# Kernel tuning notes

Hardware: AMD Instinct MI355X
Metric: run time of the kernel (lower is better)

## Reference

```python
import jax, jax.numpy as jnp
import numpy as np

H = 1024
V = 50257
L = 4096

def setup_inputs() -> dict:
    key = jax.random.key(0)
    ks = jax.random.split(key, 10)
    s = 1.0 / np.sqrt(H)
    return {
        "input": jax.random.randint(ks[0], (1,), 0, V, dtype=jnp.int64),
        "hidden": jax.random.normal(ks[1], (1, 1, H), dtype=jnp.float32),
        "encoder_hiddens": jax.random.normal(ks[2], (L, H), dtype=jnp.float32),
        "embedding": jax.random.normal(ks[3], (V, H), dtype=jnp.float32),
        "w_ih": jax.random.uniform(ks[4], (3 * H, H), minval=-s, maxval=s, dtype=jnp.float32),
        "w_hh": jax.random.uniform(ks[5], (3 * H, H), minval=-s, maxval=s, dtype=jnp.float32),
        "b_ih": jax.random.uniform(ks[6], (3 * H,), minval=-s, maxval=s, dtype=jnp.float32),
        "b_hh": jax.random.uniform(ks[7], (3 * H,), minval=-s, maxval=s, dtype=jnp.float32),
        "out_w": jax.random.uniform(ks[8], (V, 2 * H), minval=-s, maxval=s, dtype=jnp.float32),
        "out_b": jax.random.uniform(ks[9], (V,), minval=-s, maxval=s, dtype=jnp.float32),
    }


def _gru_step(x, h, w_ih, w_hh, b_ih, b_hh):
    # x, h: (H,). PyTorch GRU cell gate math (gate order: r, z, n).
    gi = w_ih @ x + b_ih                      # (3H,)
    gh = w_hh @ h + b_hh                      # (3H,)
    i_r, i_z, i_n = gi[:H], gi[H:2 * H], gi[2 * H:]
    h_r, h_z, h_n = gh[:H], gh[H:2 * H], gh[2 * H:]
    r = jax.nn.sigmoid(i_r + h_r)
    z = jax.nn.sigmoid(i_z + h_z)
    n = jnp.tanh(i_n + r * h_n)
    return (1.0 - z) * n + z * h


def reference(input, hidden, encoder_hiddens, embedding, w_ih, w_hh, b_ih, b_hh, out_w, out_b):
    # Embedding lookup of single token -> (H,); dropout is identity at inference.
    x = embedding[input].reshape(-1)
    h = hidden[0, 0]                          # (H,)
    h_new = _gru_step(x, h, w_ih, w_hh, b_ih, b_hh)  # (H,)
    # Dot-product attention over encoder hiddens (L, H)
    scores = encoder_hiddens @ h_new          # (L,)
    attn = jax.nn.softmax(scores)             # (L,)
    ctx = attn @ encoder_hiddens              # (H,)
    concat = jnp.concatenate([ctx, h_new])    # (2H,)
    logits = out_w @ concat + out_b           # (V,)
    output = jax.nn.log_softmax(logits)[None, :]  # (1, V)
    return output, h_new[None, None, :]
```

## Files before the change

kernel.cpp:

```cpp
#include <hip/hip_runtime.h>
#include <hip/hip_bf16.h>

#define H 1024
#define V 50257
#define L 4096
#define CTXB 128
#define ROWS (L / CTXB)

__device__ __forceinline__ float sigmoidf_(float x) { return 1.f / (1.f + expf(-x)); }

__device__ __forceinline__ float dot4(float4 w, float4 c) {
    return w.x * c.x + w.y * c.y + w.z * c.z + w.w * c.w;
}

__global__ __launch_bounds__(64) void k_gru(const int* __restrict__ idx,
        const float* __restrict__ hidden, const float* __restrict__ emb,
        const float* __restrict__ w_ih, const float* __restrict__ w_hh,
        const float* __restrict__ b_ih, const float* __restrict__ b_hh,
        float* __restrict__ concat, float* __restrict__ out_h) {
    const int j = blockIdx.x;
    const int lane = threadIdx.x;
    const float* x   = emb + (size_t)idx[0] * H;
    const float* wir = w_ih + (size_t)j * H;
    const float* wiz = wir + (size_t)H * H;
    const float* win = wiz + (size_t)H * H;
    const float* whr = w_hh + (size_t)j * H;
    const float* whz = whr + (size_t)H * H;
    const float* whn = whz + (size_t)H * H;
    float sir = 0, siz = 0, sin_ = 0, shr = 0, shz = 0, shn = 0;
    #pragma unroll
    for (int it = 0; it < 4; ++it) {
        int elem = (it * 64 + lane) * 4;
        float4 xf = *(const float4*)(x + elem);
        float4 hf = *(const float4*)(hidden + elem);
        sir  += dot4(*(const float4*)(wir + elem), xf);
        siz  += dot4(*(const float4*)(wiz + elem), xf);
        sin_ += dot4(*(const float4*)(win + elem), xf);
        shr  += dot4(*(const float4*)(whr + elem), hf);
        shz  += dot4(*(const float4*)(whz + elem), hf);
        shn  += dot4(*(const float4*)(whn + elem), hf);
    }
    #pragma unroll
    for (int off = 32; off; off >>= 1) {
        sir += __shfl_xor(sir, off); siz += __shfl_xor(siz, off);
        sin_ += __shfl_xor(sin_, off); shr += __shfl_xor(shr, off);
        shz += __shfl_xor(shz, off); shn += __shfl_xor(shn, off);
    }
    if (lane == 0) {
        float r = sigmoidf_(sir + b_ih[j]       + shr + b_hh[j]);
        float z = sigmoidf_(siz + b_ih[H + j]   + shz + b_hh[H + j]);
        float n = tanhf(sin_ + b_ih[2*H + j] + r * (shn + b_hh[2*H + j]));
        float hn = (1.f - z) * n + z * hidden[j];
        concat[H + j] = hn;
        out_h[j] = hn;
    }
}

__global__ __launch_bounds__(256) void k_scores(const float* __restrict__ enc,
        const float* __restrict__ concat, float* __restrict__ scores) {
    const int wave = threadIdx.x >> 6, lane = threadIdx.x & 63;
    const int l = blockIdx.x * 4 + wave;
    const float* row = enc + (size_t)l * H;
    const float* h = concat + H;
    float s = 0.f;
    #pragma unroll
    for (int it = 0; it < 4; ++it) {
        int elem = (it * 64 + lane) * 4;
        s += dot4(*(const float4*)(row + elem), *(const float4*)(h + elem));
    }
    #pragma unroll
    for (int off = 32; off; off >>= 1) s += __shfl_xor(s, off);
    if (lane == 0) scores[l] = s;
}

__global__ __launch_bounds__(256) void k_softmax(const float* __restrict__ scores,
                                                 float* __restrict__ attn) {
    __shared__ float sm[8];
    const int t = threadIdx.x, lane = t & 63, wave = t >> 6;
    float v[16];
    float m = -INFINITY;
    #pragma unroll
    for (int i = 0; i < 16; ++i) { v[i] = scores[i * 256 + t]; m = fmaxf(m, v[i]); }
    #pragma unroll
    for (int off = 32; off; off >>= 1) m = fmaxf(m, __shfl_xor(m, off));
    if (lane == 0) sm[wave] = m;
    __syncthreads();
    m = fmaxf(fmaxf(sm[0], sm[1]), fmaxf(sm[2], sm[3]));
    float s = 0.f;
    #pragma unroll
    for (int i = 0; i < 16; ++i) { v[i] = expf(v[i] - m); s += v[i]; }
    #pragma unroll
    for (int off = 32; off; off >>= 1) s += __shfl_xor(s, off);
    __syncthreads();
    if (lane == 0) sm[wave] = s;
    __syncthreads();
    s = sm[0] + sm[1] + sm[2] + sm[3];
    float inv = 1.f / s;
    #pragma unroll
    for (int i = 0; i < 16; ++i) attn[i * 256 + t] = v[i] * inv;
}

__global__ __launch_bounds__(256) void k_ctx_partial(const float* __restrict__ enc,
        const float* __restrict__ attn, float* __restrict__ partial) {
    __shared__ float a[ROWS];
    const int t = threadIdx.x;
    const int r0 = blockIdx.x * ROWS;
    if (t < ROWS) a[t] = attn[r0 + t];
    __syncthreads();
    float acc0 = 0, acc1 = 0, acc2 = 0, acc3 = 0;
    const float* p = enc + (size_t)r0 * H + t * 4;
    #pragma unroll
    for (int l0 = 0; l0 < ROWS; l0 += 8) {
        float4 w[8];
        #pragma unroll
        for (int k = 0; k < 8; ++k) w[k] = *(const float4*)(p + (size_t)(l0 + k) * H);
        #pragma unroll
        for (int k = 0; k < 8; ++k) {
            float al = a[l0 + k];
            acc0 += al * w[k].x; acc1 += al * w[k].y;
            acc2 += al * w[k].z; acc3 += al * w[k].w;
        }
    }
    *(float4*)(partial + (size_t)blockIdx.x * H + t * 4) = make_float4(acc0, acc1, acc2, acc3);
}

__global__ __launch_bounds__(256) void k_ctx_reduce(const float* __restrict__ partial,
                                                    float* __restrict__ concat) {
    const int c = blockIdx.x * 256 + threadIdx.x;
    float s = 0.f;
    for (int p = 0; p < CTXB; ++p) s += partial[(size_t)p * H + c];
    concat[c] = s;
}

__global__ __launch_bounds__(256) void k_logits(const float* __restrict__ out_w,
        const float* __restrict__ out_b, const float* __restrict__ concat,
        float* __restrict__ logits) {
    const int wave = threadIdx.x >> 6, lane = threadIdx.x & 63;
    const int v = blockIdx.x * 4 + wave;
    if (v >= V) return;
    const float* row = out_w + (size_t)v * (2 * H);
    float s = 0.f;
    #pragma unroll
    for (int it = 0; it < 8; ++it) {
        int elem = (it * 64 + lane) * 4;
        s += dot4(*(const float4*)(row + elem), *(const float4*)(concat + elem));
    }
    #pragma unroll
    for (int off = 32; off; off >>= 1) s += __shfl_xor(s, off);
    if (lane == 0) logits[v] = s + out_b[v];
}

__global__ __launch_bounds__(256) void k_lse_partial(const float* __restrict__ logits,
                                                     float* __restrict__ red) {
    __shared__ float sm[4], ss[4];
    const int t = threadIdx.x;
    const int i = blockIdx.x * 256 + t;
    float m = -INFINITY, s = 0.f;
    for (int v = i; v < V; v += 64 * 256) {
        float x = logits[v];
        float M = fmaxf(m, x);
        s = s * expf(m - M) + expf(x - M);
        m = M;
    }
    const int lane = t & 63, wave = t >> 6;
    #pragma unroll
    for (int off = 32; off; off >>= 1) {
        float m2 = __shfl_xor(m, off), s2 = __shfl_xor(s, off);
        float M = fmaxf(m, m2);
        s = s * expf(m - M) + s2 * expf(m2 - M);
        m = M;
    }
    if (lane == 0) { sm[wave] = m; ss[wave] = s; }
    __syncthreads();
    if (t == 0) {
        float M = fmaxf(fmaxf(sm[0], sm[1]), fmaxf(sm[2], sm[3]));
        float S = ss[0] * expf(sm[0] - M) + ss[1] * expf(sm[1] - M) +
                  ss[2] * expf(sm[2] - M) + ss[3] * expf(sm[3] - M);
        red[blockIdx.x] = M;
        red[64 + blockIdx.x] = S;
    }
}

__global__ __launch_bounds__(256) void k_write(const float* __restrict__ logits,
        const float* __restrict__ red, float* __restrict__ out) {
    __shared__ float sC;
    const int t = threadIdx.x;
    if (t < 64) {
        float m = red[t], s = red[64 + t];
        #pragma unroll
        for (int off = 32; off; off >>= 1) {
            float m2 = __shfl_xor(m, off), s2 = __shfl_xor(s, off);
            float M = fmaxf(m, m2);
            s = s * expf(m - M) + s2 * expf(m2 - M);
            m = M;
        }
        if (t == 0) sC = m + logf(s);
    }
    __syncthreads();
    const float C = sC;
    const int v = blockIdx.x * 256 + t;
    if (v < V) out[v] = logits[v] - C;
}

extern "C" void kernel_launch(void* const* d_in, const int* in_sizes, int n_in,
                              void* d_out, int out_size, void* d_ws, size_t ws_size,
                              hipStream_t stream) {
    const int*   idx    = (const int*)d_in[0];
    const float* hidden = (const float*)d_in[1];
    const float* enc    = (const float*)d_in[2];
    const float* emb    = (const float*)d_in[3];
    const float* w_ih   = (const float*)d_in[4];
    const float* w_hh   = (const float*)d_in[5];
    const float* b_ih   = (const float*)d_in[6];
    const float* b_hh   = (const float*)d_in[7];
    const float* out_w  = (const float*)d_in[8];
    const float* out_b  = (const float*)d_in[9];
    float* out = (float*)d_out;

    float* ws      = (float*)d_ws;
    float* concat  = ws;
    float* scores  = ws + 2048;
    float* attn    = ws + 6144;
    float* partial = ws + 10240;
    float* logits  = ws + 141312;
    float* red     = ws + 191584;

    k_gru<<<H, 64, 0, stream>>>(idx, hidden, emb, w_ih, w_hh, b_ih, b_hh, concat, out + V);
    k_scores<<<L / 4, 256, 0, stream>>>(enc, concat, scores);
    k_softmax<<<1, 256, 0, stream>>>(scores, attn);
    k_ctx_partial<<<CTXB, 256, 0, stream>>>(enc, attn, partial);
    k_ctx_reduce<<<4, 256, 0, stream>>>(partial, concat);
    k_logits<<<(V + 3) / 4, 256, 0, stream>>>(out_w, out_b, concat, logits);
    k_lse_partial<<<64, 256, 0, stream>>>(logits, red);
    k_write<<<(V + 255) / 256, 256, 0, stream>>>(logits, red, out);
}
```

Baseline: 659.5 us.

## Fuse decoder step into one persistent cooperative kernel with grid syncs

The eight separate kernels (GRU, attention scores, softmax, context partial and reduce, logits, LSE partial, write) become one cooperative kernel of 256 blocks by 512 threads, with grid.sync between stages. The intent is to remove per-launch overhead and inter-kernel gaps. The logits pass also gains a per-wave online max/sum, so no separate pass is needed to compute log-sum-exp. The trade-off is lower occupancy, since the persistent grid has only 8 waves per block and each wave loops over many out_w rows, which may limit memory-level parallelism on the dominant output-projection stream.

```diff
diff --git a/kernel.cpp b/kernel.cpp
--- a/kernel.cpp
+++ b/kernel.cpp
@@ -1,11 +1,16 @@
 #include <hip/hip_runtime.h>
-#include <hip/hip_bf16.h>
+#include <hip/hip_cooperative_groups.h>
+
+namespace cg = cooperative_groups;
 
 #define H 1024
 #define V 50257
 #define L 4096
-#define CTXB 128
-#define ROWS (L / CTXB)
+#define NB 256
+#define NT 512
+#define NW 8
+#define GWAVES (NB * NW)
+#define ROWS2 (L / NB)
 
 __device__ __forceinline__ float sigmoidf_(float x) { return 1.f / (1.f + expf(-x)); }
 
@@ -13,193 +18,238 @@
     return w.x * c.x + w.y * c.y + w.z * c.z + w.w * c.w;
 }
 
-__global__ __launch_bounds__(64) void k_gru(const int* __restrict__ idx,
-        const float* __restrict__ hidden, const float* __restrict__ emb,
+__global__ __launch_bounds__(NT, 1) void k_mega(
+        const int* __restrict__ idx, const float* __restrict__ hidden,
+        const float* __restrict__ enc, const float* __restrict__ emb,
         const float* __restrict__ w_ih, const float* __restrict__ w_hh,
         const float* __restrict__ b_ih, const float* __restrict__ b_hh,
-        float* __restrict__ concat, float* __restrict__ out_h) {
-    const int j = blockIdx.x;
-    const int lane = threadIdx.x;
-    const float* x   = emb + (size_t)idx[0] * H;
-    const float* wir = w_ih + (size_t)j * H;
-    const float* wiz = wir + (size_t)H * H;
-    const float* win = wiz + (size_t)H * H;
-    const float* whr = w_hh + (size_t)j * H;
-    const float* whz = whr + (size_t)H * H;
-    const float* whn = whz + (size_t)H * H;
-    float sir = 0, siz = 0, sin_ = 0, shr = 0, shz = 0, shn = 0;
-    #pragma unroll
-    for (int it = 0; it < 4; ++it) {
-        int elem = (it * 64 + lane) * 4;
-        float4 xf = *(const float4*)(x + elem);
-        float4 hf = *(const float4*)(hidden + elem);
-        sir  += dot4(*(const float4*)(wir + elem), xf);
-        siz  += dot4(*(const float4*)(wiz + elem), xf);
-        sin_ += dot4(*(const float4*)(win + elem), xf);
-        shr  += dot4(*(const float4*)(whr + elem), hf);
-        shz  += dot4(*(const float4*)(whz + elem), hf);
-        shn  += dot4(*(const float4*)(whn + elem), hf);
-    }
-    #pragma unroll
-    for (int off = 32; off; off >>= 1) {
-        sir += __shfl_xor(sir, off); siz += __shfl_xor(siz, off);
-        sin_ += __shfl_xor(sin_, off); shr += __shfl_xor(shr, off);
-        shz += __shfl_xor(shz, off); shn += __shfl_xor(shn, off);
-    }
-    if (lane == 0) {
+        const float* __restrict__ out_w, const float* __restrict__ out_b,
+        float* __restrict__ out, float* __restrict__ ws) {
+    cg::grid_group grid = cg::this_grid();
+    const int t = threadIdx.x;
+    const int w = t >> 6, lane = t & 63;
+    const int bid = blockIdx.x;
+    const int gw = bid * NW + w;
+
+    float* concat  = ws;
+    float* scores  = ws + 2048;
+    float* Sb      = ws + 6144;
+    float* bmax    = ws + 6400;
+    float* red     = ws + 6656;
+    float* partial = ws + 8192;
+    float* logits  = ws + 8192 + NB * H;
+
+    __shared__ float gpart[NW][6];
+    __shared__ float wmax_s[NW];
+    __shared__ float eL[ROWS2];
+    __shared__ float aL[ROWS2];
+    __shared__ float mw[NW], sw[NW];
+    __shared__ float sScalar;
+
+    {
+        const int j = bid * 4 + (w >> 1);
+        const int half = w & 1;
+        const float* x   = emb + (size_t)idx[0] * H;
+        const float* wir = w_ih + (size_t)j * H;
+        const float* wiz = wir + (size_t)H * H;
+        const float* win = wiz + (size_t)H * H;
+        const float* whr = w_hh + (size_t)j * H;
+        const float* whz = whr + (size_t)H * H;
+        const float* whn = whz + (size_t)H * H;
+        float sir = 0, siz = 0, sin_ = 0, shr = 0, shz = 0, shn = 0;
+        #pragma unroll
+        for (int it = 0; it < 2; ++it) {
+            int elem = half * 512 + (it * 64 + lane) * 4;
+            float4 xf = *(const float4*)(x + elem);
+            float4 hf = *(const float4*)(hidden + elem);
+            sir  += dot4(*(const float4*)(wir + elem), xf);
+            siz  += dot4(*(const float4*)(wiz + elem), xf);
+            sin_ += dot4(*(const float4*)(win + elem), xf);
+            shr  += dot4(*(const float4*)(whr + elem), hf);
+            shz  += dot4(*(const float4*)(whz + elem), hf);
+            shn  += dot4(*(const float4*)(whn + elem), hf);
+        }
+        #pragma unroll
+        for (int off = 32; off; off >>= 1) {
+            sir += __shfl_xor(sir, off); siz += __shfl_xor(siz, off);
+            sin_ += __shfl_xor(sin_, off); shr += __shfl_xor(shr, off);
+            shz += __shfl_xor(shz, off); shn += __shfl_xor(shn, off);
+        }
+        if (lane == 0) {
+            gpart[w][0] = sir; gpart[w][1] = siz; gpart[w][2] = sin_;
+            gpart[w][3] = shr; gpart[w][4] = shz; gpart[w][5] = shn;
+        }
+    }
+    __syncthreads();
+    if (lane == 0 && (w & 1) == 0) {
+        const int j = bid * 4 + (w >> 1);
+        float sir = gpart[w][0] + gpart[w + 1][0];
+        float siz = gpart[w][1] + gpart[w + 1][1];
+        float sin_ = gpart[w][2] + gpart[w + 1][2];
+        float shr = gpart[w][3] + gpart[w + 1][3];
+        float shz = gpart[w][4] + gpart[w + 1][4];
+        float shn = gpart[w][5] + gpart[w + 1][5];
         float r = sigmoidf_(sir + b_ih[j]       + shr + b_hh[j]);
         float z = sigmoidf_(siz + b_ih[H + j]   + shz + b_hh[H + j]);
-        float n = tanhf(sin_ + b_ih[2*H + j] + r * (shn + b_hh[2*H + j]));
+        float n = tanhf(sin_ + b_ih[2 * H + j] + r * (shn + b_hh[2 * H + j]));
         float hn = (1.f - z) * n + z * hidden[j];
         concat[H + j] = hn;
-        out_h[j] = hn;
-    }
-}
-
-__global__ __launch_bounds__(256) void k_scores(const float* __restrict__ enc,
-        const float* __restrict__ concat, float* __restrict__ scores) {
-    const int wave = threadIdx.x >> 6, lane = threadIdx.x & 63;
-    const int l = blockIdx.x * 4 + wave;
-    const float* row = enc + (size_t)l * H;
-    const float* h = concat + H;
-    float s = 0.f;
-    #pragma unroll
-    for (int it = 0; it < 4; ++it) {
-        int elem = (it * 64 + lane) * 4;
-        s += dot4(*(const float4*)(row + elem), *(const float4*)(h + elem));
-    }
-    #pragma unroll
-    for (int off = 32; off; off >>= 1) s += __shfl_xor(s, off);
-    if (lane == 0) scores[l] = s;
-}
-
-__global__ __launch_bounds__(256) void k_softmax(const float* __restrict__ scores,
-                                                 float* __restrict__ attn) {
-    __shared__ float sm[8];
-    const int t = threadIdx.x, lane = t & 63, wave = t >> 6;
-    float v[16];
-    float m = -INFINITY;
-    #pragma unroll
-    for (int i = 0; i < 16; ++i) { v[i] = scores[i * 256 + t]; m = fmaxf(m, v[i]); }
-    #pragma unroll
-    for (int off = 32; off; off >>= 1) m = fmaxf(m, __shfl_xor(m, off));
-    if (lane == 0) sm[wave] = m;
-    __syncthreads();
-    m = fmaxf(fmaxf(sm[0], sm[1]), fmaxf(sm[2], sm[3]));
-    float s = 0.f;
-    #pragma unroll
-    for (int i = 0; i < 16; ++i) { v[i] = expf(v[i] - m); s += v[i]; }
-    #pragma unroll
-    for (int off = 32; off; off >>= 1) s += __shfl_xor(s, off);
-    __syncthreads();
-    if (lane == 0) sm[wave] = s;
-    __syncthreads();
-    s = sm[0] + sm[1] + sm[2] + sm[3];
-    float inv = 1.f / s;
-    #pragma unroll
-    for (int i = 0; i < 16; ++i) attn[i * 256 + t] = v[i] * inv;
-}
-
-__global__ __launch_bounds__(256) void k_ctx_partial(const float* __restrict__ enc,
-        const float* __restrict__ attn, float* __restrict__ partial) {
-    __shared__ float a[ROWS];
-    const int t = threadIdx.x;
-    const int r0 = blockIdx.x * ROWS;
-    if (t < ROWS) a[t] = attn[r0 + t];
-    __syncthreads();
-    float acc0 = 0, acc1 = 0, acc2 = 0, acc3 = 0;
-    const float* p = enc + (size_t)r0 * H + t * 4;
-    #pragma unroll
-    for (int l0 = 0; l0 < ROWS; l0 += 8) {
-        float4 w[8];
-        #pragma unroll
-        for (int k = 0; k < 8; ++k) w[k] = *(const float4*)(p + (size_t)(l0 + k) * H);
-        #pragma unroll
-        for (int k = 0; k < 8; ++k) {
-            float al = a[l0 + k];
-            acc0 += al * w[k].x; acc1 += al * w[k].y;
-            acc2 += al * w[k].z; acc3 += al * w[k].w;
-        }
-    }
-    *(float4*)(partial + (size_t)blockIdx.x * H + t * 4) = make_float4(acc0, acc1, acc2, acc3);
-}
-
-__global__ __launch_bounds__(256) void k_ctx_reduce(const float* __restrict__ partial,
-                                                    float* __restrict__ concat) {
-    const int c = blockIdx.x * 256 + threadIdx.x;
-    float s = 0.f;
-    for (int p = 0; p < CTXB; ++p) s += partial[(size_t)p * H + c];
-    concat[c] = s;
-}
-
-__global__ __launch_bounds__(256) void k_logits(const float* __restrict__ out_w,
-        const float* __restrict__ out_b, const float* __restrict__ concat,
-        float* __restrict__ logits) {
-    const int wave = threadIdx.x >> 6, lane = threadIdx.x & 63;
-    const int v = blockIdx.x * 4 + wave;
-    if (v >= V) return;
-    const float* row = out_w + (size_t)v * (2 * H);
-    float s = 0.f;
-    #pragma unroll
-    for (int it = 0; it < 8; ++it) {
-        int elem = (it * 64 + lane) * 4;
-        s += dot4(*(const float4*)(row + elem), *(const float4*)(concat + elem));
-    }
-    #pragma unroll
-    for (int off = 32; off; off >>= 1) s += __shfl_xor(s, off);
-    if (lane == 0) logits[v] = s + out_b[v];
-}
-
-__global__ __launch_bounds__(256) void k_lse_partial(const float* __restrict__ logits,
-                                                     float* __restrict__ red) {
-    __shared__ float sm[4], ss[4];
-    const int t = threadIdx.x;
-    const int i = blockIdx.x * 256 + t;
-    float m = -INFINITY, s = 0.f;
-    for (int v = i; v < V; v += 64 * 256) {
-        float x = logits[v];
-        float M = fmaxf(m, x);
-        s = s * expf(m - M) + expf(x - M);
-        m = M;
-    }
-    const int lane = t & 63, wave = t >> 6;
-    #pragma unroll
-    for (int off = 32; off; off >>= 1) {
-        float m2 = __shfl_xor(m, off), s2 = __shfl_xor(s, off);
-        float M = fmaxf(m, m2);
-        s = s * expf(m - M) + s2 * expf(m2 - M);
-        m = M;
-    }
-    if (lane == 0) { sm[wave] = m; ss[wave] = s; }
+        out[V + j] = hn;
+    }
+    grid.sync();
+
+    {
+        const float* h = concat + H;
+        float wmax = -INFINITY;
+        #pragma unroll
+        for (int r = 0; r < 2; ++r) {
+            const int l = gw + r * GWAVES;
+            const float* row = enc + (size_t)l * H;
+            float s = 0.f;
+            #pragma unroll
+            for (int it = 0; it < 4; ++it) {
+                int elem = (it * 64 + lane) * 4;
+                s += dot4(*(const float4*)(row + elem), *(const float4*)(h + elem));
+            }
+            #pragma unroll
+            for (int off = 32; off; off >>= 1) s += __shfl_xor(s, off);
+            if (lane == 0) scores[l] = s;
+            wmax = fmaxf(wmax, s);
+        }
+        if (lane == 0) wmax_s[w] = wmax;
+    }
     __syncthreads();
     if (t == 0) {
-        float M = fmaxf(fmaxf(sm[0], sm[1]), fmaxf(sm[2], sm[3]));
-        float S = ss[0] * expf(sm[0] - M) + ss[1] * expf(sm[1] - M) +
-                  ss[2] * expf(sm[2] - M) + ss[3] * expf(sm[3] - M);
-        red[blockIdx.x] = M;
-        red[64 + blockIdx.x] = S;
-    }
-}
-
-__global__ __launch_bounds__(256) void k_write(const float* __restrict__ logits,
-        const float* __restrict__ red, float* __restrict__ out) {
-    __shared__ float sC;
-    const int t = threadIdx.x;
-    if (t < 64) {
-        float m = red[t], s = red[64 + t];
+        float m = wmax_s[0];
+        #pragma unroll
+        for (int k = 1; k < NW; ++k) m = fmaxf(m, wmax_s[k]);
+        bmax[bid] = m;
+    }
+    grid.sync();
+
+    if (w == 0) {
+        float m = fmaxf(fmaxf(bmax[lane], bmax[lane + 64]),
+                        fmaxf(bmax[lane + 128], bmax[lane + 192]));
+        #pragma unroll
+        for (int off = 32; off; off >>= 1) m = fmaxf(m, __shfl_xor(m, off));
+        if (lane == 0) sScalar = m;
+    }
+    __syncthreads();
+    {
+        const float M = sScalar;
+        const int r0 = bid * ROWS2;
+        if (t < ROWS2) eL[t] = expf(scores[r0 + t] - M);
+    }
+    __syncthreads();
+    if (t == 0) {
+        float s = 0.f;
+        #pragma unroll
+        for (int k = 0; k < ROWS2; ++k) s += eL[k];
+        Sb[bid] = s;
+    }
+    grid.sync();
+
+    if (w == 0) {
+        float s = Sb[lane] + Sb[lane + 64] + Sb[lane + 128] + Sb[lane + 192];
+        #pragma unroll
+        for (int off = 32; off; off >>= 1) s += __shfl_xor(s, off);
+        if (lane == 0) sScalar = s;
+    }
+    __syncthreads();
+    {
+        const float invS = 1.f / sScalar;
+        if (t < ROWS2) aL[t] = eL[t] * invS;
+    }
+    __syncthreads();
+    {
+        const int r0 = bid * ROWS2;
+        float2 acc = make_float2(0.f, 0.f);
+        const float* pbase = enc + (size_t)r0 * H + 2 * t;
+        #pragma unroll
+        for (int l = 0; l < ROWS2; ++l) {
+            float2 v = *(const float2*)(pbase + (size_t)l * H);
+            float a = aL[l];
+            acc.x += a * v.x; acc.y += a * v.y;
+        }
+        *(float2*)(partial + (size_t)bid * H + 2 * t) = acc;
+    }
+    grid.sync();
+
+    if (w < 4) {
+        const int c = bid * 4 + w;
+        float s = 0.f;
+        #pragma unroll
+        for (int k = 0; k < 4; ++k)
+            s += partial[(size_t)(lane + 64 * k) * H + c];
+        #pragma unroll
+        for (int off = 32; off; off >>= 1) s += __shfl_xor(s, off);
+        if (lane == 0) concat[c] = s;
+    }
+    grid.sync();
+
+    {
+        float4 cv[8];
+        #pragma unroll
+        for (int it = 0; it < 8; ++it)
+            cv[it] = *(const float4*)(concat + (it * 64 + lane) * 4);
+        float lm = -INFINITY, ls = 0.f;
+        for (int v = gw; v < V; v += GWAVES) {
+            const float* row = out_w + (size_t)v * (2 * H);
+            float s = 0.f;
+            #pragma unroll
+            for (int it = 0; it < 8; ++it) {
+                int elem = (it * 64 + lane) * 4;
+                s += dot4(*(const float4*)(row + elem), cv[it]);
+            }
+            #pragma unroll
+            for (int off = 32; off; off >>= 1) s += __shfl_xor(s, off);
+            s += out_b[v];
+            if (lane == 0) logits[v] = s;
+            float Mn = fmaxf(lm, s);
+            ls = ls * expf(lm - Mn) + expf(s - Mn);
+            lm = Mn;
+        }
+        if (lane == 0) { mw[w] = lm; sw[w] = ls; }
+    }
+    __syncthreads();
+    if (t == 0) {
+        float m = mw[0], s = sw[0];
+        #pragma unroll
+        for (int k = 1; k < NW; ++k) {
+            float Mn = fmaxf(m, mw[k]);
+            s = s * expf(m - Mn) + sw[k] * expf(mw[k] - Mn);
+            m = Mn;
+        }
+        red[bid] = m;
+        red[NB + bid] = s;
+    }
+    grid.sync();
+
+    if (w == 0) {
+        float m = -INFINITY, s = 0.f;
+        #pragma unroll
+        for (int k = 0; k < 4; ++k) {
+            int i = lane + 64 * k;
+            float m2 = red[i], s2 = red[NB + i];
+            float Mn = fmaxf(m, m2);
+            s = s * expf(m - Mn) + s2 * expf(m2 - Mn);
+            m = Mn;
+        }
         #pragma unroll
         for (int off = 32; off; off >>= 1) {
             float m2 = __shfl_xor(m, off), s2 = __shfl_xor(s, off);
-            float M = fmaxf(m, m2);
-            s = s * expf(m - M) + s2 * expf(m2 - M);
-            m = M;
-        }
-        if (t == 0) sC = m + logf(s);
-    }
-    __syncthreads();
-    const float C = sC;
-    const int v = blockIdx.x * 256 + t;
-    if (v < V) out[v] = logits[v] - C;
+            float Mn = fmaxf(m, m2);
+            s = s * expf(m - Mn) + s2 * expf(m2 - Mn);
+            m = Mn;
+        }
+        if (lane == 0) sScalar = m + logf(s);
+    }
+    __syncthreads();
+    {
+        const float C = sScalar;
+        const int v = bid * NT + t;
+        if (v < V) out[v] = logits[v] - C;
+    }
 }
 
 extern "C" void kernel_launch(void* const* d_in, const int* in_sizes, int n_in,
@@ -216,21 +266,10 @@
     const float* out_w  = (const float*)d_in[8];
     const float* out_b  = (const float*)d_in[9];
     float* out = (float*)d_out;
-
-    float* ws      = (float*)d_ws;
-    float* concat  = ws;
-    float* scores  = ws + 2048;
-    float* attn    = ws + 6144;
-    float* partial = ws + 10240;
-    float* logits  = ws + 141312;
-    float* red     = ws + 191584;
-
-    k_gru<<<H, 64, 0, stream>>>(idx, hidden, emb, w_ih, w_hh, b_ih, b_hh, concat, out + V);
-    k_scores<<<L / 4, 256, 0, stream>>>(enc, concat, scores);
-    k_softmax<<<1, 256, 0, stream>>>(scores, attn);
-    k_ctx_partial<<<CTXB, 256, 0, stream>>>(enc, attn, partial);
-    k_ctx_reduce<<<4, 256, 0, stream>>>(partial, concat);
-    k_logits<<<(V + 3) / 4, 256, 0, stream>>>(out_w, out_b, concat, logits);
-    k_lse_partial<<<64, 256, 0, stream>>>(logits, red);
-    k_write<<<(V + 255) / 256, 256, 0, stream>>>(logits, red, out);
+    float* ws  = (float*)d_ws;
+
+    void* args[] = { (void*)&idx, (void*)&hidden, (void*)&enc, (void*)&emb,
+                     (void*)&w_ih, (void*)&w_hh, (void*)&b_ih, (void*)&b_hh,
+                     (void*)&out_w, (void*)&out_b, (void*)&out, (void*)&ws };
+    hipLaunchCooperativeKernel((void*)k_mega, dim3(NB), dim3(NT), args, 0, stream);
 }
```

Result: slower. 834.3 us (+26.5%).

## Fuse softmax into scores/ctx via atomic max, fold LSE into logits kernel

Applied to the files above, without the earlier changes.

Drops the separate attention-softmax and LSE-partial kernels. Score blocks publish a global max through an order-preserving atomicMax key, and the context kernel computes the exponentials and per-block sums itself; normalisation is applied in the reduce step. The logits kernel now uses a grid-stride loop with concat cached in registers and computes an online max/sum, and the GRU kernel splits each row across two waves. This saves launches and the single-block softmax bottleneck, at the cost of an atomic and a larger partial reduction (256 blocks).

```diff
diff --git a/kernel.cpp b/kernel.cpp
--- a/kernel.cpp
+++ b/kernel.cpp
@@ -1,11 +1,8 @@
 #include <hip/hip_runtime.h>
-#include <hip/hip_bf16.h>
 
 #define H 1024
 #define V 50257
 #define L 4096
-#define CTXB 128
-#define ROWS (L / CTXB)
 
 __device__ __forceinline__ float sigmoidf_(float x) { return 1.f / (1.f + expf(-x)); }
 
@@ -13,13 +10,25 @@
     return w.x * c.x + w.y * c.y + w.z * c.z + w.w * c.w;
 }
 
-__global__ __launch_bounds__(64) void k_gru(const int* __restrict__ idx,
+__device__ __forceinline__ unsigned int fkey(float f) {
+    unsigned int u = __float_as_uint(f);
+    return (u & 0x80000000u) ? ~u : (u | 0x80000000u);
+}
+__device__ __forceinline__ float finv(unsigned int k) {
+    return (k & 0x80000000u) ? __uint_as_float(k & 0x7FFFFFFFu) : __uint_as_float(~k);
+}
+
+__global__ __launch_bounds__(256) void k_gru(const int* __restrict__ idx,
         const float* __restrict__ hidden, const float* __restrict__ emb,
         const float* __restrict__ w_ih, const float* __restrict__ w_hh,
         const float* __restrict__ b_ih, const float* __restrict__ b_hh,
-        float* __restrict__ concat, float* __restrict__ out_h) {
-    const int j = blockIdx.x;
-    const int lane = threadIdx.x;
+        float* __restrict__ concat, float* __restrict__ out_h,
+        unsigned int* __restrict__ gmax) {
+    __shared__ float gpart[4][6];
+    const int t = threadIdx.x, w = t >> 6, lane = t & 63;
+    const int j = blockIdx.x * 2 + (w >> 1);
+    const int half = w & 1;
+    if (blockIdx.x == 0 && t == 0) *gmax = 0u;
     const float* x   = emb + (size_t)idx[0] * H;
     const float* wir = w_ih + (size_t)j * H;
     const float* wiz = wir + (size_t)H * H;
@@ -29,8 +38,8 @@
     const float* whn = whz + (size_t)H * H;
     float sir = 0, siz = 0, sin_ = 0, shr = 0, shz = 0, shn = 0;
     #pragma unroll
-    for (int it = 0; it < 4; ++it) {
-        int elem = (it * 64 + lane) * 4;
+    for (int it = 0; it < 2; ++it) {
+        int elem = half * 512 + (it * 64 + lane) * 4;
         float4 xf = *(const float4*)(x + elem);
         float4 hf = *(const float4*)(hidden + elem);
         sir  += dot4(*(const float4*)(wir + elem), xf);
@@ -47,9 +56,20 @@
         shz += __shfl_xor(shz, off); shn += __shfl_xor(shn, off);
     }
     if (lane == 0) {
-        float r = sigmoidf_(sir + b_ih[j]       + shr + b_hh[j]);
-        float z = sigmoidf_(siz + b_ih[H + j]   + shz + b_hh[H + j]);
-        float n = tanhf(sin_ + b_ih[2*H + j] + r * (shn + b_hh[2*H + j]));
+        gpart[w][0] = sir; gpart[w][1] = siz; gpart[w][2] = sin_;
+        gpart[w][3] = shr; gpart[w][4] = shz; gpart[w][5] = shn;
+    }
+    __syncthreads();
+    if (lane == 0 && half == 0) {
+        float a0 = gpart[w][0] + gpart[w + 1][0];
+        float a1 = gpart[w][1] + gpart[w + 1][1];
+        float a2 = gpart[w][2] + gpart[w + 1][2];
+        float a3 = gpart[w][3] + gpart[w + 1][3];
+        float a4 = gpart[w][4] + gpart[w + 1][4];
+        float a5 = gpart[w][5] + gpart[w + 1][5];
+        float r = sigmoidf_(a0 + b_ih[j]       + a3 + b_hh[j]);
+        float z = sigmoidf_(a1 + b_ih[H + j]   + a4 + b_hh[H + j]);
+        float n = tanhf(a2 + b_ih[2 * H + j] + r * (a5 + b_hh[2 * H + j]));
         float hn = (1.f - z) * n + z * hidden[j];
         concat[H + j] = hn;
         out_h[j] = hn;
@@ -57,9 +77,11 @@
 }
 
 __global__ __launch_bounds__(256) void k_scores(const float* __restrict__ enc,
-        const float* __restrict__ concat, float* __restrict__ scores) {
-    const int wave = threadIdx.x >> 6, lane = threadIdx.x & 63;
-    const int l = blockIdx.x * 4 + wave;
+        const float* __restrict__ concat, float* __restrict__ scores,
+        unsigned int* __restrict__ gmax) {
+    __shared__ float wm[4];
+    const int w = threadIdx.x >> 6, lane = threadIdx.x & 63;
+    const int l = blockIdx.x * 4 + w;
     const float* row = enc + (size_t)l * H;
     const float* h = concat + H;
     float s = 0.f;
@@ -70,134 +92,124 @@
     }
     #pragma unroll
     for (int off = 32; off; off >>= 1) s += __shfl_xor(s, off);
-    if (lane == 0) scores[l] = s;
-}
-
-__global__ __launch_bounds__(256) void k_softmax(const float* __restrict__ scores,
-                                                 float* __restrict__ attn) {
-    __shared__ float sm[8];
-    const int t = threadIdx.x, lane = t & 63, wave = t >> 6;
-    float v[16];
-    float m = -INFINITY;
-    #pragma unroll
-    for (int i = 0; i < 16; ++i) { v[i] = scores[i * 256 + t]; m = fmaxf(m, v[i]); }
-    #pragma unroll
-    for (int off = 32; off; off >>= 1) m = fmaxf(m, __shfl_xor(m, off));
-    if (lane == 0) sm[wave] = m;
-    __syncthreads();
-    m = fmaxf(fmaxf(sm[0], sm[1]), fmaxf(sm[2], sm[3]));
-    float s = 0.f;
-    #pragma unroll
-    for (int i = 0; i < 16; ++i) { v[i] = expf(v[i] - m); s += v[i]; }
-    #pragma unroll
-    for (int off = 32; off; off >>= 1) s += __shfl_xor(s, off);
-    __syncthreads();
-    if (lane == 0) sm[wave] = s;
-    __syncthreads();
-    s = sm[0] + sm[1] + sm[2] + sm[3];
-    float inv = 1.f / s;
-    #pragma unroll
-    for (int i = 0; i < 16; ++i) attn[i * 256 + t] = v[i] * inv;
+    if (lane == 0) { scores[l] = s; wm[w] = s; }
+    __syncthreads();
+    if (threadIdx.x == 0) {
+        float m = fmaxf(fmaxf(wm[0], wm[1]), fmaxf(wm[2], wm[3]));
+        atomicMax(gmax, fkey(m));
+    }
 }
 
 __global__ __launch_bounds__(256) void k_ctx_partial(const float* __restrict__ enc,
-        const float* __restrict__ attn, float* __restrict__ partial) {
-    __shared__ float a[ROWS];
+        const float* __restrict__ scores, const unsigned int* __restrict__ gmax,
+        float* __restrict__ partial, float* __restrict__ sb) {
+    __shared__ float eL[16];
     const int t = threadIdx.x;
-    const int r0 = blockIdx.x * ROWS;
-    if (t < ROWS) a[t] = attn[r0 + t];
-    __syncthreads();
+    const int r0 = blockIdx.x * 16;
+    if (t < 16) eL[t] = expf(scores[r0 + t] - finv(*gmax));
+    __syncthreads();
+    if (t == 0) {
+        float s = 0.f;
+        #pragma unroll
+        for (int k = 0; k < 16; ++k) s += eL[k];
+        sb[blockIdx.x] = s;
+    }
     float acc0 = 0, acc1 = 0, acc2 = 0, acc3 = 0;
     const float* p = enc + (size_t)r0 * H + t * 4;
     #pragma unroll
-    for (int l0 = 0; l0 < ROWS; l0 += 8) {
-        float4 w[8];
-        #pragma unroll
-        for (int k = 0; k < 8; ++k) w[k] = *(const float4*)(p + (size_t)(l0 + k) * H);
-        #pragma unroll
-        for (int k = 0; k < 8; ++k) {
-            float al = a[l0 + k];
-            acc0 += al * w[k].x; acc1 += al * w[k].y;
-            acc2 += al * w[k].z; acc3 += al * w[k].w;
-        }
+    for (int l = 0; l < 16; ++l) {
+        float4 v = *(const float4*)(p + (size_t)l * H);
+        float e = eL[l];
+        acc0 += e * v.x; acc1 += e * v.y; acc2 += e * v.z; acc3 += e * v.w;
     }
     *(float4*)(partial + (size_t)blockIdx.x * H + t * 4) = make_float4(acc0, acc1, acc2, acc3);
 }
 
 __global__ __launch_bounds__(256) void k_ctx_reduce(const float* __restrict__ partial,
-                                                    float* __restrict__ concat) {
-    const int c = blockIdx.x * 256 + threadIdx.x;
-    float s = 0.f;
-    for (int p = 0; p < CTXB; ++p) s += partial[(size_t)p * H + c];
-    concat[c] = s;
+        const float* __restrict__ sb, float* __restrict__ concat) {
+    __shared__ float sS[4];
+    const int t = threadIdx.x, w = t >> 6, lane = t & 63;
+    float s = sb[t];
+    #pragma unroll
+    for (int off = 32; off; off >>= 1) s += __shfl_xor(s, off);
+    if (lane == 0) sS[w] = s;
+    __syncthreads();
+    const float invS = 1.f / (sS[0] + sS[1] + sS[2] + sS[3]);
+    const int c = blockIdx.x * 256 + t;
+    float acc = 0.f;
+    #pragma unroll 8
+    for (int b = 0; b < 256; ++b) acc += partial[(size_t)b * H + c];
+    concat[c] = acc * invS;
 }
 
 __global__ __launch_bounds__(256) void k_logits(const float* __restrict__ out_w,
         const float* __restrict__ out_b, const float* __restrict__ concat,
-        float* __restrict__ logits) {
-    const int wave = threadIdx.x >> 6, lane = threadIdx.x & 63;
-    const int v = blockIdx.x * 4 + wave;
-    if (v >= V) return;
-    const float* row = out_w + (size_t)v * (2 * H);
-    float s = 0.f;
-    #pragma unroll
-    for (int it = 0; it < 8; ++it) {
-        int elem = (it * 64 + lane) * 4;
-        s += dot4(*(const float4*)(row + elem), *(const float4*)(concat + elem));
-    }
-    #pragma unroll
-    for (int off = 32; off; off >>= 1) s += __shfl_xor(s, off);
-    if (lane == 0) logits[v] = s + out_b[v];
-}
-
-__global__ __launch_bounds__(256) void k_lse_partial(const float* __restrict__ logits,
-                                                     float* __restrict__ red) {
-    __shared__ float sm[4], ss[4];
-    const int t = threadIdx.x;
-    const int i = blockIdx.x * 256 + t;
+        float* __restrict__ logits, float* __restrict__ red) {
+    __shared__ float mw[4], sw[4];
+    const int w = threadIdx.x >> 6, lane = threadIdx.x & 63;
+    const int gw = blockIdx.x * 4 + w;
+    float4 cv[8];
+    #pragma unroll
+    for (int it = 0; it < 8; ++it)
+        cv[it] = *(const float4*)(concat + (it * 64 + lane) * 4);
+    float lm = -INFINITY, ls = 0.f;
+    for (int v = gw; v < V; v += 8192) {
+        const float* row = out_w + (size_t)v * (2 * H);
+        float s = 0.f;
+        #pragma unroll
+        for (int it = 0; it < 8; ++it) {
+            int elem = (it * 64 + lane) * 4;
+            s += dot4(*(const float4*)(row + elem), cv[it]);
+        }
+        #pragma unroll
+        for (int off = 32; off; off >>= 1) s += __shfl_xor(s, off);
+        s += out_b[v];
+        if (lane == 0) logits[v] = s;
+        float Mn = fmaxf(lm, s);
+        ls = ls * expf(lm - Mn) + expf(s - Mn);
+        lm = Mn;
+    }
+    if (lane == 0) { mw[w] = lm; sw[w] = ls; }
+    __syncthreads();
+    if (threadIdx.x == 0) {
+        float m = mw[0], s = sw[0];
+        #pragma unroll
+        for (int k = 1; k < 4; ++k) {
+            float Mn = fmaxf(m, mw[k]);
+            s = s * expf(m - Mn) + sw[k] * expf(mw[k] - Mn);
+            m = Mn;
+        }
+        red[blockIdx.x] = m;
+        red[2048 + blockIdx.x] = s;
+    }
+}
+
+__global__ __launch_bounds__(256) void k_write(const float* __restrict__ logits,
+        const float* __restrict__ red, float* __restrict__ out) {
+    __shared__ float smv[4], ssv[4];
+    const int t = threadIdx.x, w = t >> 6, lane = t & 63;
     float m = -INFINITY, s = 0.f;
-    for (int v = i; v < V; v += 64 * 256) {
-        float x = logits[v];
-        float M = fmaxf(m, x);
-        s = s * expf(m - M) + expf(x - M);
-        m = M;
-    }
-    const int lane = t & 63, wave = t >> 6;
+    #pragma unroll
+    for (int k = 0; k < 8; ++k) {
+        int i = t * 8 + k;
+        float m2 = red[i], s2 = red[2048 + i];
+        float Mn = fmaxf(m, m2);
+        s = s * expf(m - Mn) + s2 * expf(m2 - Mn);
+        m = Mn;
+    }
     #pragma unroll
     for (int off = 32; off; off >>= 1) {
         float m2 = __shfl_xor(m, off), s2 = __shfl_xor(s, off);
-        float M = fmaxf(m, m2);
-        s = s * expf(m - M) + s2 * expf(m2 - M);
-        m = M;
-    }
-    if (lane == 0) { sm[wave] = m; ss[wave] = s; }
-    __syncthreads();
-    if (t == 0) {
-        float M = fmaxf(fmaxf(sm[0], sm[1]), fmaxf(sm[2], sm[3]));
-        float S = ss[0] * expf(sm[0] - M) + ss[1] * expf(sm[1] - M) +
-                  ss[2] * expf(sm[2] - M) + ss[3] * expf(sm[3] - M);
-        red[blockIdx.x] = M;
-        red[64 + blockIdx.x] = S;
-    }
-}
-
-__global__ __launch_bounds__(256) void k_write(const float* __restrict__ logits,
-        const float* __restrict__ red, float* __restrict__ out) {
-    __shared__ float sC;
-    const int t = threadIdx.x;
-    if (t < 64) {
-        float m = red[t], s = red[64 + t];
-        #pragma unroll
-        for (int off = 32; off; off >>= 1) {
-            float m2 = __shfl_xor(m, off), s2 = __shfl_xor(s, off);
-            float M = fmaxf(m, m2);
-            s = s * expf(m - M) + s2 * expf(m2 - M);
-            m = M;
-        }
-        if (t == 0) sC = m + logf(s);
-    }
-    __syncthreads();
-    const float C = sC;
+        float Mn = fmaxf(m, m2);
+        s = s * expf(m - Mn) + s2 * expf(m2 - Mn);
+        m = Mn;
+    }
+    if (lane == 0) { smv[w] = m; ssv[w] = s; }
+    __syncthreads();
+    float M = fmaxf(fmaxf(smv[0], smv[1]), fmaxf(smv[2], smv[3]));
+    float S = ssv[0] * expf(smv[0] - M) + ssv[1] * expf(smv[1] - M) +
+              ssv[2] * expf(smv[2] - M) + ssv[3] * expf(smv[3] - M);
+    const float C = M + logf(S);
     const int v = blockIdx.x * 256 + t;
     if (v < V) out[v] = logits[v] - C;
 }
@@ -220,17 +232,17 @@
     float* ws      = (float*)d_ws;
     float* concat  = ws;
     float* scores  = ws + 2048;
-    float* attn    = ws + 6144;
-    float* partial = ws + 10240;
-    float* logits  = ws + 141312;
-    float* red     = ws + 191584;
-
-    k_gru<<<H, 64, 0, stream>>>(idx, hidden, emb, w_ih, w_hh, b_ih, b_hh, concat, out + V);
-    k_scores<<<L / 4, 256, 0, stream>>>(enc, concat, scores);
-    k_softmax<<<1, 256, 0, stream>>>(scores, attn);
-    k_ctx_partial<<<CTXB, 256, 0, stream>>>(enc, attn, partial);
-    k_ctx_reduce<<<4, 256, 0, stream>>>(partial, concat);
-    k_logits<<<(V + 3) / 4, 256, 0, stream>>>(out_w, out_b, concat, logits);
-    k_lse_partial<<<64, 256, 0, stream>>>(logits, red);
+    float* sb      = ws + 6144;
+    unsigned int* gmax = (unsigned int*)(ws + 6400);
+    float* red     = ws + 6656;
+    float* partial = ws + 16384;
+    float* logits  = ws + 278528;
+
+    k_gru<<<512, 256, 0, stream>>>(idx, hidden, emb, w_ih, w_hh, b_ih, b_hh,
+                                   concat, out + V, gmax);
+    k_scores<<<L / 4, 256, 0, stream>>>(enc, concat, scores, gmax);
+    k_ctx_partial<<<256, 256, 0, stream>>>(enc, scores, gmax, partial, sb);
+    k_ctx_reduce<<<4, 256, 0, stream>>>(partial, sb, concat);
+    k_logits<<<2048, 256, 0, stream>>>(out_w, out_b, concat, logits, red);
     k_write<<<(V + 255) / 256, 256, 0, stream>>>(logits, red, out);
 }
```

After: 675.6 us. 1.02x slower.
